# Optimization experiments

Hardware: AMD Instinct MI355X
Metric: run time of the kernel (lower is better)

The kernel has to match this reference:

```python
import jax, jax.numpy as jnp
import numpy as np
from jax import lax

BLOCK_SPECS = [(32, 64, 1), (64, 128, 2), (128, 128, 1)]  # (cin, cout, stride)
EPS = 1e-5


def _bn(x, gamma, beta):
    # training-mode BatchNorm2d: batch statistics over (N, H, W), biased var
    m = x.mean(axis=(0, 2, 3), keepdims=True)
    v = x.var(axis=(0, 2, 3), keepdims=True)
    return gamma[None, :, None, None] * (x - m) * lax.rsqrt(v + EPS) + beta[None, :, None, None]


def _dwsep(x, dw_w, dw_b, g1, be1, pw_w, pw_b, g2, be2, stride):
    C = x.shape[1]
    # fused depthwise conv (equivalent to the per-channel Conv2d(1,1,3) loop)
    y = lax.conv_general_dilated(x, dw_w, (stride, stride), ((1, 1), (1, 1)),
                                 feature_group_count=C,
                                 dimension_numbers=('NCHW', 'OIHW', 'NCHW'))
    y = y + dw_b[None, :, None, None]
    y = jax.nn.relu(_bn(y, g1, be1))
    # pointwise 1x1 conv
    y = jnp.einsum('bchw,oc->bohw', y, pw_w) + pw_b[None, :, None, None]
    return jax.nn.relu(_bn(y, g2, be2))


def setup_inputs() -> dict:
    key = jax.random.key(0)
    ks = jax.random.split(key, 1 + 8 * len(BLOCK_SPECS))
    d = {"x": jax.random.normal(ks[0], (32, 32, 112, 112), dtype=jnp.float32)}
    i = 1
    for b, (cin, cout, st) in enumerate(BLOCK_SPECS):
        d[f"b{b}_dw_w"] = 0.1 * jax.random.normal(ks[i], (cin, 1, 3, 3), jnp.float32); i += 1
        d[f"b{b}_dw_b"] = 0.01 * jax.random.normal(ks[i], (cin,), jnp.float32); i += 1
        d[f"b{b}_g1"] = 1.0 + 0.1 * jax.random.normal(ks[i], (cin,), jnp.float32); i += 1
        d[f"b{b}_be1"] = 0.01 * jax.random.normal(ks[i], (cin,), jnp.float32); i += 1
        d[f"b{b}_pw_w"] = 0.1 * jax.random.normal(ks[i], (cout, cin), jnp.float32); i += 1
        d[f"b{b}_pw_b"] = 0.01 * jax.random.normal(ks[i], (cout,), jnp.float32); i += 1
        d[f"b{b}_g2"] = 1.0 + 0.1 * jax.random.normal(ks[i], (cout,), jnp.float32); i += 1
        d[f"b{b}_be2"] = 0.01 * jax.random.normal(ks[i], (cout,), jnp.float32); i += 1
    return d


def reference(x,
              b0_dw_w, b0_dw_b, b0_g1, b0_be1, b0_pw_w, b0_pw_b, b0_g2, b0_be2,
              b1_dw_w, b1_dw_b, b1_g1, b1_be1, b1_pw_w, b1_pw_b, b1_g2, b1_be2,
              b2_dw_w, b2_dw_b, b2_g1, b2_be1, b2_pw_w, b2_pw_b, b2_g2, b2_be2):
    blocks = [
        (b0_dw_w, b0_dw_b, b0_g1, b0_be1, b0_pw_w, b0_pw_b, b0_g2, b0_be2),
        (b1_dw_w, b1_dw_b, b1_g1, b1_be1, b1_pw_w, b1_pw_b, b1_g2, b1_be2),
        (b2_dw_w, b2_dw_b, b2_g1, b2_be1, b2_pw_w, b2_pw_b, b2_g2, b2_be2),
    ]
    y = x
    for (_, _, st), p in zip(BLOCK_SPECS, blocks):
        y = _dwsep(y, *p, stride=st)
    # final AvgPool2d over the whole remaining spatial map -> [B, C, 1, 1]
    return y.mean(axis=(2, 3), keepdims=True)
```

## Files before the change

kernel.cpp:

```cpp
#include <hip/hip_runtime.h>

#define EPSV 1e-5f
#define NBINS 32

typedef unsigned short u16;
typedef unsigned int u32;
typedef __attribute__((ext_vector_type(4))) unsigned short ush4;
typedef __attribute__((ext_vector_type(8))) unsigned short ush8;
typedef __attribute__((ext_vector_type(8))) short short8;
typedef __attribute__((ext_vector_type(4))) float f32x4;

__device__ __forceinline__ float relu(float x) { return fmaxf(x, 0.f); }

__device__ __forceinline__ u16 f2bf(float f) {
    u32 u = __builtin_bit_cast(u32, f);
    u32 r = (u + 0x7fffu + ((u >> 16) & 1u)) >> 16;
    return (u16)r;
}
__device__ __forceinline__ float bf2f(u16 v) {
    return __builtin_bit_cast(float, (u32)v << 16);
}

template<int CIN, int COUT>
__device__ __forceinline__ void prep_one(const float* __restrict__ w,
                                         u16* __restrict__ dst, int widx) {
    const int NT = COUT / 16;
    int lane = widx & 63;
    int t  = (widx >> 6) % NT;
    int ks = (widx >> 6) / NT;
    int co  = t * 16 + (lane & 15);
    int ci0 = ks * 32 + (lane >> 4) * 8;
#pragma unroll
    for (int i = 0; i < 8; i++)
        dst[(size_t)widx * 8 + i] = f2bf(w[co * CIN + ci0 + i]);
}

__global__ void prep_k(const float* __restrict__ w0, const float* __restrict__ w1,
                       const float* __restrict__ w2, u16* __restrict__ s0,
                       u16* __restrict__ s1, u16* __restrict__ s2,
                       float* __restrict__ bins) {
    int i = blockIdx.x * 256 + threadIdx.x;
    for (int z = i; z < 6 * 2 * NBINS * 128; z += 3328) bins[z] = 0.f;
    if (i < 256)       prep_one<32, 64>  (w0, s0, i);
    else if (i < 1280) prep_one<64, 128> (w1, s1, i - 256);
    else if (i < 3328) prep_one<128, 128>(w2, s2, i - 1280);
}

template<int IHW, int C, bool BNIN, int BR, int LST, typename TIN>
__global__ __launch_bounds__(256) void dwlds_k(
    const TIN* __restrict__ in, u16* __restrict__ out,
    const float* __restrict__ w9, const float* __restrict__ bias,
    const float* __restrict__ gamma, const float* __restrict__ beta,
    const float* __restrict__ bsum_in, const float* __restrict__ bsq_in,
    float invcnt_in, float* __restrict__ bsum, float* __restrict__ bsq)
{
    constexpr bool F32 = sizeof(TIN) == 4;
    constexpr int NB  = IHW / BR;
    constexpr int TPR = IHW / 8;
    constexpr int NACT = BR * TPR;
    constexpr int W4 = IHW / 4;
    __shared__ float tile[(BR + 2) * LST];
    __shared__ float bnss[2];
    __shared__ float redbuf[8];

    const int bid = blockIdx.x;
    const int plane = bid / NB;
    const int band  = bid % NB;
    const int c = plane & (C - 1);
    const int tid = threadIdx.x;

    if (BNIN) {
        if (tid < NBINS) {
            float s = bsum_in[tid * C + c];
            float q = bsq_in [tid * C + c];
#pragma unroll
            for (int m = NBINS / 2; m >= 1; m >>= 1) {
                s += __shfl_xor(s, m); q += __shfl_xor(q, m);
            }
            if (tid == 0) {
                float mm  = s * invcnt_in;
                float var = fmaf(q, invcnt_in, -mm * mm);
                float is  = gamma[c] * rsqrtf(var + EPSV);
                bnss[0] = is; bnss[1] = fmaf(-mm, is, beta[c]);
            }
        }
        __syncthreads();
    }
    const float scv = BNIN ? bnss[0] : 1.f;
    const float shv = BNIN ? bnss[1] : 0.f;

    const int r0 = band * BR;
    const TIN* base = in + (size_t)plane * (IHW * IHW);

    for (int i = tid; i < (BR + 2) * 2; i += 256) {
        int r = i >> 1, side = i & 1;
        float4 z = {0.f, 0.f, 0.f, 0.f};
        *(float4*)&tile[r * LST + side * (IHW + 4)] = z;
    }
    for (int i = tid; i < (BR + 2) * W4; i += 256) {
        int r = i / W4, c4 = (i % W4) * 4;
        int gr = r0 - 1 + r;
        float4 v = {0.f, 0.f, 0.f, 0.f};
        if (gr >= 0 && gr < IHW) {
            if constexpr (F32) {
                v = *(const float4*)(base + (size_t)gr * IHW + c4);
            } else {
                ush4 h = *(const ush4*)(base + (size_t)gr * IHW + c4);
                v = {bf2f(h[0]), bf2f(h[1]), bf2f(h[2]), bf2f(h[3])};
            }
            if (BNIN) {
                v.x = relu(fmaf(v.x, scv, shv)); v.y = relu(fmaf(v.y, scv, shv));
                v.z = relu(fmaf(v.z, scv, shv)); v.w = relu(fmaf(v.w, scv, shv));
            }
        }
        *(float4*)&tile[r * LST + 4 + c4] = v;
    }
    __syncthreads();

    float s = 0.f, q = 0.f;
    if (tid < NACT) {
        const int r  = tid / TPR;
        const int c0 = (tid % TPR) * 8;
        float wv[9];
#pragma unroll
        for (int k = 0; k < 9; k++) wv[k] = w9[c * 9 + k];
        float bz = bias[c];
        float a[8];
#pragma unroll
        for (int j = 0; j < 8; j++) a[j] = bz;
#pragma unroll
        for (int kr = 0; kr < 3; kr++) {
            const float* rp = &tile[(r + kr) * LST + 3 + c0];
            float v[10];
#pragma unroll
            for (int i = 0; i < 10; i++) v[i] = rp[i];
#pragma unroll
            for (int j = 0; j < 8; j++)
                a[j] = fmaf(wv[kr * 3], v[j],
                        fmaf(wv[kr * 3 + 1], v[j + 1],
                         fmaf(wv[kr * 3 + 2], v[j + 2], a[j])));
        }
        u16* ob = out + (size_t)plane * (IHW * IHW) + (size_t)(r0 + r) * IHW + c0;
        ush4 o0 = {f2bf(a[0]), f2bf(a[1]), f2bf(a[2]), f2bf(a[3])};
        ush4 o1 = {f2bf(a[4]), f2bf(a[5]), f2bf(a[6]), f2bf(a[7])};
        *(ush4*)ob = o0;
        *(ush4*)(ob + 4) = o1;
#pragma unroll
        for (int j = 0; j < 8; j++) { s += a[j]; q = fmaf(a[j], a[j], q); }
    }
#pragma unroll
    for (int m = 32; m >= 1; m >>= 1) { s += __shfl_xor(s, m); q += __shfl_xor(q, m); }
    int lane = tid & 63, wid = tid >> 6;
    if (lane == 0) { redbuf[wid] = s; redbuf[4 + wid] = q; }
    __syncthreads();
    if (tid == 0) {
        s = redbuf[0] + redbuf[1] + redbuf[2] + redbuf[3];
        q = redbuf[4] + redbuf[5] + redbuf[6] + redbuf[7];
        unsigned bin = bid & (NBINS - 1);
        atomicAdd(&bsum[bin * C + c], s);
        atomicAdd(&bsq [bin * C + c], q);
    }
}

template<int IHW, int OHW, int C, int G>
__global__ __launch_bounds__(256) void dwtile2_k(
    const u16* __restrict__ in, u16* __restrict__ out,
    const float* __restrict__ w9, const float* __restrict__ bias,
    const float* __restrict__ gamma, const float* __restrict__ beta,
    const float* __restrict__ bsum_in, const float* __restrict__ bsq_in,
    float invcnt_in, float* __restrict__ bsum, float* __restrict__ bsq)
{
    constexpr int S = 2;
    constexpr int CT = OHW / 4;
    constexpr int TPP = CT * CT;
    __shared__ float lsc[C], lsh[C];

    const int tid = threadIdx.x;
    for (int cc = tid; cc < C; cc += 256) {
        float s = 0.f, q = 0.f;
        for (int b = 0; b < NBINS; b++) {
            s += bsum_in[b * C + cc];
            q += bsq_in [b * C + cc];
        }
        float mm  = s * invcnt_in;
        float var = fmaf(q, invcnt_in, -mm * mm);
        float is  = gamma[cc] * rsqrtf(var + EPSV);
        lsc[cc] = is; lsh[cc] = fmaf(-mm, is, beta[cc]);
    }
    __syncthreads();

    int t = blockIdx.x * 256 + tid;
    int plane = t / TPP;
    int w = t % TPP;
    int rt = w / CT, ct = w % CT;
    int c = plane & (C - 1);

    const u16* base = in + (size_t)plane * (IHW * IHW);
    const float scv = lsc[c], shv = lsh[c];
    float wv[9];
#pragma unroll
    for (int k = 0; k < 9; k++) wv[k] = w9[c * 9 + k];
    float bz = bias[c];

    float acc[4][4];
#pragma unroll
    for (int j = 0; j < 4; j++)
#pragma unroll
        for (int cc = 0; cc < 4; cc++) acc[j][cc] = bz;

    const int r0 = rt * 4;
    const int icb = ct * 4 * S;

    auto T = [&](float v) { return relu(fmaf(v, scv, shv)); };

#pragma unroll
    for (int rin = 0; rin < 9; rin++) {
        int ih = r0 * S + rin - 1;
        if (ih < 0 || ih >= IHW) continue;
        const u16* rp = base + (size_t)ih * IHW;
        float sq[9];
        ush4 M = *(const ush4*)(rp + icb);
        ush4 R = *(const ush4*)(rp + icb + 4);
#pragma unroll
        for (int i = 0; i < 4; i++) { sq[1 + i] = T(bf2f(M[i])); sq[5 + i] = T(bf2f(R[i])); }
        sq[0] = (icb > 0) ? T(bf2f(rp[icb - 1])) : 0.f;
#pragma unroll
        for (int j = 0; j < 4; j++) {
            int kh = rin - S * j;
            if (kh < 0 || kh > 2) continue;
#pragma unroll
            for (int cc = 0; cc < 4; cc++)
#pragma unroll
                for (int kw = 0; kw < 3; kw++)
                    acc[j][cc] = fmaf(wv[kh * 3 + kw], sq[S * cc + kw], acc[j][cc]);
        }
    }

    u16* ob = out + (size_t)plane * (OHW * OHW) + (size_t)r0 * OHW + ct * 4;
    float s = 0.f, q = 0.f;
#pragma unroll
    for (int j = 0; j < 4; j++) {
        ush4 o;
#pragma unroll
        for (int cc = 0; cc < 4; cc++) {
            float v = acc[j][cc];
            o[cc] = f2bf(v);
            s += v;
            q = fmaf(v, v, q);
        }
        *(ush4*)(ob + (size_t)j * OHW) = o;
    }
#pragma unroll
    for (int m = G / 2; m >= 1; m >>= 1) { s += __shfl_xor(s, m); q += __shfl_xor(q, m); }
    if ((tid & (G - 1)) == 0) {
        unsigned bin = blockIdx.x & (NBINS - 1);
        atomicAdd(&bsum[bin * C + c], s);
        atomicAdd(&bsq [bin * C + c], q);
    }
}

template<int CIN, int COUT, int HW>
__global__ __launch_bounds__(256, 4) void pwmfma_k(
    const u16* __restrict__ in, u16* __restrict__ out,
    const u16* __restrict__ wswz, const float* __restrict__ bias,
    const float* __restrict__ gamma, const float* __restrict__ beta,
    const float* __restrict__ bsum_in, const float* __restrict__ bsq_in,
    float invcnt_in, float* __restrict__ bsum, float* __restrict__ bsq)
{
    constexpr int NK = CIN / 32;
    constexpr int NT = COUT / 16;
    constexpr int ROWSTRIDE = NK * 512 + 8;
    __shared__ u16 frag[4 * ROWSTRIDE];
    __shared__ float lsum[4 * COUT];
    __shared__ float lsq [4 * COUT];
    __shared__ float scs[CIN], shs[CIN];

    const int tid = threadIdx.x;

    if (tid < CIN) {
        float s = 0.f, q = 0.f;
        for (int b = 0; b < NBINS; b++) {
            s += bsum_in[b * CIN + tid];
            q += bsq_in [b * CIN + tid];
        }
        float mm  = s * invcnt_in;
        float var = fmaf(q, invcnt_in, -mm * mm);
        float is  = gamma[tid] * rsqrtf(var + EPSV);
        scs[tid] = is; shs[tid] = fmaf(-mm, is, beta[tid]);
    }
    __syncthreads();

    const size_t pixbase = (size_t)blockIdx.x * 64;
    const int n  = (int)(pixbase / HW);
    const int p0 = (int)(pixbase % HW);

    {
        const int px = tid & 63;
        const int kq = tid >> 6;
        const u16* ipx = in + (size_t)n * CIN * HW + p0 + px;
#pragma unroll
        for (int ks = 0; ks < NK; ks++) {
            const int ci0 = (ks * 4 + kq) * 8;
            short8 pkd;
#pragma unroll
            for (int j = 0; j < 8; j++) {
                float v = relu(fmaf(bf2f(ipx[(size_t)(ci0 + j) * HW]), scs[ci0 + j], shs[ci0 + j]));
                pkd[j] = (short)f2bf(v);
            }
            *(short8*)&frag[(size_t)(px >> 4) * ROWSTRIDE + ks * 512 + ((px & 15) + 16 * kq) * 8] = pkd;
        }
    }
    __syncthreads();

    const int wv   = tid >> 6;
    const int lane = tid & 63;
    f32x4 acc[NT];
#pragma unroll
    for (int t = 0; t < NT; t++) acc[t] = (f32x4){0.f, 0.f, 0.f, 0.f};

    const short8* wp = (const short8*)wswz;
#pragma unroll
    for (int ks = 0; ks < NK; ks++) {
        short8 af = *(const short8*)&frag[(size_t)wv * ROWSTRIDE + ks * 512 + lane * 8];
#pragma unroll
        for (int t = 0; t < NT; t++) {
            short8 bf = wp[(ks * NT + t) * 64 + lane];
            acc[t] = __builtin_amdgcn_mfma_f32_16x16x32_bf16(af, bf, acc[t], 0, 0, 0);
        }
    }

    const int col  = lane & 15;
    const int prow = (lane >> 4) * 4;
    const int p    = p0 + wv * 16 + prow;
#pragma unroll
    for (int t = 0; t < NT; t++) {
        int co = t * 16 + col;
        float bz = bias[co];
        float v0 = acc[t][0] + bz, v1 = acc[t][1] + bz;
        float v2 = acc[t][2] + bz, v3 = acc[t][3] + bz;
        ush4 o = {f2bf(v0), f2bf(v1), f2bf(v2), f2bf(v3)};
        *(ush4*)(out + ((size_t)n * COUT + co) * HW + p) = o;
        float s = (v0 + v1) + (v2 + v3);
        float q = fmaf(v0, v0, fmaf(v1, v1, fmaf(v2, v2, v3 * v3)));
        s += __shfl_xor(s, 16); q += __shfl_xor(q, 16);
        s += __shfl_xor(s, 32); q += __shfl_xor(q, 32);
        if (lane < 16) { lsum[wv * COUT + co] = s; lsq[wv * COUT + co] = q; }
    }
    __syncthreads();
    if (tid < COUT) {
        const unsigned bin = blockIdx.x & (NBINS - 1);
        float s = lsum[tid] + lsum[COUT + tid] + lsum[2 * COUT + tid] + lsum[3 * COUT + tid];
        float q = lsq[tid]  + lsq[COUT + tid]  + lsq[2 * COUT + tid]  + lsq[3 * COUT + tid];
        atomicAdd(&bsum[bin * COUT + tid], s);
        atomicAdd(&bsq [bin * COUT + tid], q);
    }
}

template<int HW, int C>
__global__ __launch_bounds__(256) void avgpool_k(
    const u16* __restrict__ t,
    const float* __restrict__ gamma, const float* __restrict__ beta,
    const float* __restrict__ bsum_in, const float* __restrict__ bsq_in,
    float invcnt_in, float* __restrict__ out)
{
    __shared__ float bnss[2];
    __shared__ float red[4];
    int nc = blockIdx.x;
    int c = nc & (C - 1);
    int tid = threadIdx.x;

    if (tid < NBINS) {
        float s = bsum_in[tid * C + c];
        float q = bsq_in [tid * C + c];
#pragma unroll
        for (int m = NBINS / 2; m >= 1; m >>= 1) { s += __shfl_xor(s, m); q += __shfl_xor(q, m); }
        if (tid == 0) {
            float mm  = s * invcnt_in;
            float var = fmaf(q, invcnt_in, -mm * mm);
            float is  = gamma[c] * rsqrtf(var + EPSV);
            bnss[0] = is; bnss[1] = fmaf(-mm, is, beta[c]);
        }
    }
    __syncthreads();
    float scv = bnss[0], shv = bnss[1];

    const u16* pl = t + (size_t)nc * HW;
    float s = 0.f;
    for (int p = tid * 8; p < HW; p += 2048) {
        ush8 v = *(const ush8*)(pl + p);
#pragma unroll
        for (int i = 0; i < 8; i++) s += relu(fmaf(bf2f(v[i]), scv, shv));
    }
    int lane = tid & 63, wid = tid >> 6;
#pragma unroll
    for (int o = 32; o; o >>= 1) s += __shfl_down(s, o);
    if (lane == 0) red[wid] = s;
    __syncthreads();
    if (tid == 0) out[nc] = (red[0] + red[1] + red[2] + red[3]) * (1.f / HW);
}

extern "C" void kernel_launch(void* const* d_in, const int* in_sizes, int n_in,
                              void* d_out, int out_size, void* d_ws, size_t ws_size,
                              hipStream_t stream)
{
    const float* x = (const float*)d_in[0];
    const float* P[3][8];
    for (int b = 0; b < 3; b++)
        for (int j = 0; j < 8; j++)
            P[b][j] = (const float*)d_in[1 + b * 8 + j];

    float* ws = (float*)d_ws;
    float* stats = ws;
    u16*  wswz0  = (u16*)(stats + 49152);
    u16*  wswz1  = wswz0 + 2048;
    u16*  wswz2  = wswz1 + 8192;
    u16*  A      = wswz2 + 16384;
    u16*  B      = A + 13000000;

    float* out = (float*)d_out;

    prep_k<<<13, 256, 0, stream>>>(P[0][4], P[1][4], P[2][4], wswz0, wswz1, wswz2, stats);

#define BSUM(i) (stats + (i) * 8192)
#define BSQ(i)  (stats + (i) * 8192 + 4096)

    const float inv1 = 1.f / (32.f * 12544.f);
    const float inv2 = 1.f / (32.f * 3136.f);

    dwlds_k<112, 32, false, 16, 120, float><<<7168, 256, 0, stream>>>(
        x, A, P[0][0], P[0][1], nullptr, nullptr, nullptr, nullptr, 0.f,
        BSUM(0), BSQ(0));

    pwmfma_k<32, 64, 12544><<<6272, 256, 0, stream>>>(
        A, B, wswz0, P[0][5], P[0][2], P[0][3], BSUM(0), BSQ(0), inv1,
        BSUM(1), BSQ(1));

    dwtile2_k<112, 56, 64, 4><<<1568, 256, 0, stream>>>(
        B, A, P[1][0], P[1][1], P[0][6], P[0][7], BSUM(1), BSQ(1), inv1,
        BSUM(2), BSQ(2));

    pwmfma_k<64, 128, 3136><<<1568, 256, 0, stream>>>(
        A, B, wswz1, P[1][5], P[1][2], P[1][3], BSUM(2), BSQ(2), inv2,
        BSUM(3), BSQ(3));

    dwlds_k<56, 128, true, 28, 68, u16><<<8192, 256, 0, stream>>>(
        B, A, P[2][0], P[2][1], P[1][6], P[1][7], BSUM(3), BSQ(3), inv2,
        BSUM(4), BSQ(4));

    pwmfma_k<128, 128, 3136><<<1568, 256, 0, stream>>>(
        A, B, wswz2, P[2][5], P[2][2], P[2][3], BSUM(4), BSQ(4), inv2,
        BSUM(5), BSQ(5));

    avgpool_k<3136, 128><<<4096, 256, 0, stream>>>(
        B, P[2][6], P[2][7], BSUM(5), BSQ(5), inv2, out);

#undef BSUM
#undef BSQ
}
```

Baseline: 180.4 us.

## Replace stride-2 depthwise register-tile kernel with LDS row-band kernel

The stride-2 depthwise conv of block 1 is rewritten so each workgroup handles one 14-output-row band of a single channel plane. The workgroup loads the 29 input rows into shared memory once, applying the previous BatchNorm and ReLU on the way in, and threads then compute 1x4 outputs from shared memory. The per-block BatchNorm finalisation is cut from a serial loop over all 64 channels to one warp-shuffle reduction for the single channel, removing a latency-heavy prologue. In exchange there are more, smaller blocks, an extra barrier and shared-memory staging, and about a quarter of the threads sit idle during compute.

```diff
diff --git a/kernel.cpp b/kernel.cpp
--- a/kernel.cpp
+++ b/kernel.cpp
@@ -162,98 +162,107 @@
     }
 }
 
-template<int IHW, int OHW, int C, int G>
-__global__ __launch_bounds__(256) void dwtile2_k(
+template<int IHW, int OHW, int C>
+__global__ __launch_bounds__(256) void dwlds2_k(
     const u16* __restrict__ in, u16* __restrict__ out,
     const float* __restrict__ w9, const float* __restrict__ bias,
     const float* __restrict__ gamma, const float* __restrict__ beta,
     const float* __restrict__ bsum_in, const float* __restrict__ bsq_in,
     float invcnt_in, float* __restrict__ bsum, float* __restrict__ bsq)
 {
-    constexpr int S = 2;
-    constexpr int CT = OHW / 4;
-    constexpr int TPP = CT * CT;
-    __shared__ float lsc[C], lsh[C];
-
+    constexpr int BRO = 14;
+    constexpr int NB  = OHW / BRO;
+    constexpr int NIR = 2 * BRO + 1;
+    constexpr int LST = 120;
+    constexpr int CT  = OHW / 4;
+    constexpr int NACT = BRO * CT;
+    constexpr int W4 = IHW / 4;
+    __shared__ float tile[NIR * LST];
+    __shared__ float bnss[2];
+    __shared__ float redbuf[8];
+
+    const int bid = blockIdx.x;
+    const int plane = bid / NB;
+    const int band  = bid % NB;
+    const int c = plane & (C - 1);
     const int tid = threadIdx.x;
-    for (int cc = tid; cc < C; cc += 256) {
-        float s = 0.f, q = 0.f;
-        for (int b = 0; b < NBINS; b++) {
-            s += bsum_in[b * C + cc];
-            q += bsq_in [b * C + cc];
-        }
-        float mm  = s * invcnt_in;
-        float var = fmaf(q, invcnt_in, -mm * mm);
-        float is  = gamma[cc] * rsqrtf(var + EPSV);
-        lsc[cc] = is; lsh[cc] = fmaf(-mm, is, beta[cc]);
-    }
-    __syncthreads();
-
-    int t = blockIdx.x * 256 + tid;
-    int plane = t / TPP;
-    int w = t % TPP;
-    int rt = w / CT, ct = w % CT;
-    int c = plane & (C - 1);
-
+
+    if (tid < NBINS) {
+        float s = bsum_in[tid * C + c];
+        float q = bsq_in [tid * C + c];
+#pragma unroll
+        for (int m = NBINS / 2; m >= 1; m >>= 1) {
+            s += __shfl_xor(s, m); q += __shfl_xor(q, m);
+        }
+        if (tid == 0) {
+            float mm  = s * invcnt_in;
+            float var = fmaf(q, invcnt_in, -mm * mm);
+            float is  = gamma[c] * rsqrtf(var + EPSV);
+            bnss[0] = is; bnss[1] = fmaf(-mm, is, beta[c]);
+        }
+    }
+    __syncthreads();
+    const float scv = bnss[0], shv = bnss[1];
+
+    const int r0 = band * BRO;
     const u16* base = in + (size_t)plane * (IHW * IHW);
-    const float scv = lsc[c], shv = lsh[c];
-    float wv[9];
-#pragma unroll
-    for (int k = 0; k < 9; k++) wv[k] = w9[c * 9 + k];
-    float bz = bias[c];
-
-    float acc[4][4];
-#pragma unroll
-    for (int j = 0; j < 4; j++)
-#pragma unroll
-        for (int cc = 0; cc < 4; cc++) acc[j][cc] = bz;
-
-    const int r0 = rt * 4;
-    const int icb = ct * 4 * S;
-
-    auto T = [&](float v) { return relu(fmaf(v, scv, shv)); };
-
-#pragma unroll
-    for (int rin = 0; rin < 9; rin++) {
-        int ih = r0 * S + rin - 1;
-        if (ih < 0 || ih >= IHW) continue;
-        const u16* rp = base + (size_t)ih * IHW;
-        float sq[9];
-        ush4 M = *(const ush4*)(rp + icb);
-        ush4 R = *(const ush4*)(rp + icb + 4);
-#pragma unroll
-        for (int i = 0; i < 4; i++) { sq[1 + i] = T(bf2f(M[i])); sq[5 + i] = T(bf2f(R[i])); }
-        sq[0] = (icb > 0) ? T(bf2f(rp[icb - 1])) : 0.f;
-#pragma unroll
-        for (int j = 0; j < 4; j++) {
-            int kh = rin - S * j;
-            if (kh < 0 || kh > 2) continue;
+
+    for (int i = tid; i < NIR; i += 256) {
+        float4 z = {0.f, 0.f, 0.f, 0.f};
+        *(float4*)&tile[i * LST] = z;
+    }
+    for (int i = tid; i < NIR * W4; i += 256) {
+        int lr = i / W4, c4 = (i % W4) * 4;
+        int gr = 2 * r0 - 1 + lr;
+        float4 v = {0.f, 0.f, 0.f, 0.f};
+        if (gr >= 0 && gr < IHW) {
+            ush4 h = *(const ush4*)(base + (size_t)gr * IHW + c4);
+            v.x = relu(fmaf(bf2f(h[0]), scv, shv));
+            v.y = relu(fmaf(bf2f(h[1]), scv, shv));
+            v.z = relu(fmaf(bf2f(h[2]), scv, shv));
+            v.w = relu(fmaf(bf2f(h[3]), scv, shv));
+        }
+        *(float4*)&tile[lr * LST + 4 + c4] = v;
+    }
+    __syncthreads();
+
+    float s = 0.f, q = 0.f;
+    if (tid < NACT) {
+        const int r  = tid / CT;
+        const int ct = tid % CT;
+        float wv[9];
+#pragma unroll
+        for (int k = 0; k < 9; k++) wv[k] = w9[c * 9 + k];
+        float bz = bias[c];
+        float a[4] = {bz, bz, bz, bz};
+#pragma unroll
+        for (int kr = 0; kr < 3; kr++) {
+            const float* rp = &tile[(2 * r + kr) * LST + 8 * ct];
+            float4 va = *(const float4*)rp;
+            float4 vb = *(const float4*)(rp + 4);
+            float4 vc = *(const float4*)(rp + 8);
+            float sq[9] = {va.w, vb.x, vb.y, vb.z, vb.w, vc.x, vc.y, vc.z, vc.w};
+            float k0 = wv[kr * 3], k1 = wv[kr * 3 + 1], k2 = wv[kr * 3 + 2];
 #pragma unroll
             for (int cc = 0; cc < 4; cc++)
-#pragma unroll
-                for (int kw = 0; kw < 3; kw++)
-                    acc[j][cc] = fmaf(wv[kh * 3 + kw], sq[S * cc + kw], acc[j][cc]);
-        }
-    }
-
-    u16* ob = out + (size_t)plane * (OHW * OHW) + (size_t)r0 * OHW + ct * 4;
-    float s = 0.f, q = 0.f;
-#pragma unroll
-    for (int j = 0; j < 4; j++) {
-        ush4 o;
-#pragma unroll
-        for (int cc = 0; cc < 4; cc++) {
-            float v = acc[j][cc];
-            o[cc] = f2bf(v);
-            s += v;
-            q = fmaf(v, v, q);
-        }
-        *(ush4*)(ob + (size_t)j * OHW) = o;
-    }
-#pragma unroll
-    for (int m = G / 2; m >= 1; m >>= 1) { s += __shfl_xor(s, m); q += __shfl_xor(q, m); }
-    if ((tid & (G - 1)) == 0) {
-        unsigned bin = blockIdx.x & (NBINS - 1);
+                a[cc] = fmaf(k0, sq[2 * cc], fmaf(k1, sq[2 * cc + 1],
+                            fmaf(k2, sq[2 * cc + 2], a[cc])));
+        }
+        u16* ob = out + (size_t)plane * (OHW * OHW) + (size_t)(r0 + r) * OHW + 4 * ct;
+        ush4 o = {f2bf(a[0]), f2bf(a[1]), f2bf(a[2]), f2bf(a[3])};
+        *(ush4*)ob = o;
+#pragma unroll
+        for (int j = 0; j < 4; j++) { s += a[j]; q = fmaf(a[j], a[j], q); }
+    }
+#pragma unroll
+    for (int m = 32; m >= 1; m >>= 1) { s += __shfl_xor(s, m); q += __shfl_xor(q, m); }
+    int lane = tid & 63, wid = tid >> 6;
+    if (lane == 0) { redbuf[wid] = s; redbuf[4 + wid] = q; }
+    __syncthreads();
+    if (tid == 0) {
+        s = redbuf[0] + redbuf[1] + redbuf[2] + redbuf[3];
+        q = redbuf[4] + redbuf[5] + redbuf[6] + redbuf[7];
+        unsigned bin = bid & (NBINS - 1);
         atomicAdd(&bsum[bin * C + c], s);
         atomicAdd(&bsq [bin * C + c], q);
     }
@@ -435,7 +444,7 @@
         A, B, wswz0, P[0][5], P[0][2], P[0][3], BSUM(0), BSQ(0), inv1,
         BSUM(1), BSQ(1));
 
-    dwtile2_k<112, 56, 64, 4><<<1568, 256, 0, stream>>>(
+    dwlds2_k<112, 56, 64><<<8192, 256, 0, stream>>>(
         B, A, P[1][0], P[1][1], P[0][6], P[0][7], BSUM(1), BSQ(1), inv1,
         BSUM(2), BSQ(2));
 
```

Measured after the change: 182.5 us. About the same (+1.1%).
